# Kernel optimization log

Measured on AMD Instinct MI355X. Metric: run time of the kernel, lower is better.

The kernel has to match this reference:

```python
import jax, jax.numpy as jnp
import numpy as np

NUM_HEADS = 8
MASK_RATE = 0.5


def setup_inputs() -> dict:
    key = jax.random.key(0)
    ks = jax.random.split(key, 6)
    B, N, C = 8, 1024, 256
    TABLE = 10
    att_embedding = jax.random.normal(ks[0], (B, N, C), dtype=jnp.float32)
    relation_position = jax.random.randint(ks[1], (B, N, N), 0, TABLE, dtype=jnp.int32)
    rel_len = jax.random.randint(ks[2], (B,), 0, 20, dtype=jnp.int32)
    W_qkv = jax.random.normal(ks[3], (C, 3 * C), dtype=jnp.float32) * (1.0 / np.sqrt(C))
    W_proj = jax.random.normal(ks[4], (C, C), dtype=jnp.float32) * (1.0 / np.sqrt(C))
    b_proj = jnp.zeros((C,), dtype=jnp.float32)
    bias_table = jax.random.normal(ks[5], (TABLE, NUM_HEADS), dtype=jnp.float32) * 0.02
    return {
        "att_embedding": att_embedding,
        "relation_position": relation_position,
        "rel_len": rel_len,
        "W_qkv": W_qkv,
        "W_proj": W_proj,
        "b_proj": b_proj,
        "bias_table": bias_table,
    }


def reference(att_embedding, relation_position, rel_len, W_qkv, W_proj, b_proj, bias_table):
    B, N, C = att_embedding.shape
    H = NUM_HEADS
    hd = C // H
    scale = hd ** -0.5

    # QKV projection (no bias): [B,N,3C] -> q,k,v each [B,H,N,hd]
    qkv = (att_embedding @ W_qkv).reshape(B, N, 3, H, hd)
    qkv = jnp.transpose(qkv, (2, 0, 3, 1, 4))
    q, k, v = qkv[0], qkv[1], qkv[2]

    # Attention scores [B,H,N,N]
    attn = jnp.einsum("bhnd,bhmd->bhnm", q, k) * scale

    # Relative position bias: gather [B,N,N,H] -> [B,H,N,N]
    pos_bias = jnp.transpose(bias_table[relation_position], (0, 3, 1, 2))

    # Mask bias: table row t gets -100 iff t > mask_len (mask_len+1 .. TABLE-1);
    # identical across heads -> compute as [B,1,N,N] instead of materializing [B,H,N,N].
    mask_len = (rel_len.astype(jnp.float32) * MASK_RATE).astype(jnp.int32)
    mask_bias = jnp.where(relation_position > mask_len[:, None, None], -100.0, 0.0)[:, None]

    attn = jax.nn.softmax(attn + pos_bias + mask_bias, axis=-1)

    # Weighted values -> [B,N,C] -> output projection
    x = jnp.einsum("bhnm,bhmd->bnhd", attn, v).reshape(B, N, C)
    x = x @ W_proj + b_proj
    return x
```

## Files before the change

kernel.cpp:

```cpp
#include <hip/hip_runtime.h>
#include <hip/hip_bf16.h>

typedef __bf16 bf16;
typedef __bf16 bf16x2 __attribute__((ext_vector_type(2)));
typedef __bf16 bf16x8 __attribute__((ext_vector_type(8)));
typedef float f32x4 __attribute__((ext_vector_type(4)));
typedef int i32x4 __attribute__((ext_vector_type(4)));

#define B_ 8
#define N_ 1024
#define C_ 256
#define H_ 8
#define C3_ 768
#define SCALE 0.17677669529663689f
#define FMAX 16.0f


__global__ __launch_bounds__(256) void prep(
    const float* __restrict__ Wqkv, const float* __restrict__ Wproj,
    bf16* __restrict__ Wq_tiled, bf16* __restrict__ Wp_tiled)
{
  int o = blockIdx.x * 256 + threadIdx.x;
  if (blockIdx.x < 768) {
    int k = o / C3_, n = o % C3_;
    float v = Wqkv[o];
    int kt = k >> 5, kk = k & 31, nt = n >> 6, nr = n & 63;
    Wq_tiled[kt * 24576 + nt * 2048 + nr * 32 + kk] = (bf16)v;
  } else {
    int p = o - 768 * 256;
    int k = p >> 8, n = p & 255;
    float v = Wproj[p];
    Wp_tiled[(k >> 5) * 8192 + n * 32 + (k & 31)] = (bf16)v;
  }
}

__global__ __launch_bounds__(256) void gemm_qkv(
    const float* __restrict__ A, const bf16* __restrict__ Wq_tiled,
    bf16* __restrict__ q, bf16* __restrict__ kT, bf16* __restrict__ vT)
{
  __shared__ bf16 As[128][40];
  __shared__ bf16 Bts[128][40];
  __shared__ bf16 Vls[64][136];

  int tid = threadIdx.x;
  int wave = tid >> 6, lane = tid & 63, quad = lane >> 4, l16 = lane & 15;
  int m0 = blockIdx.x * 128, n0 = blockIdx.y * 128;
  int msub = (wave & 1) * 64, nsub = (wave >> 1) * 64;

  f32x4 acc[4][4] = {};

  int arow = tid >> 1, akc = (tid & 1) * 16;
  const float* aptr = A + (long)(m0 + arow) * C_ + akc;
  int bn = tid >> 1, bkc = (tid & 1) * 16;
  const bf16* bptr = Wq_tiled +
      ((long)(blockIdx.y * 2 + (bn >> 6)) * 2048 + (bn & 63) * 32 + bkc);

  float4 a0 = *reinterpret_cast<const float4*>(aptr);
  float4 a1 = *reinterpret_cast<const float4*>(aptr + 4);
  float4 a2 = *reinterpret_cast<const float4*>(aptr + 8);
  float4 a3 = *reinterpret_cast<const float4*>(aptr + 12);
  i32x4 bv0 = *reinterpret_cast<const i32x4*>(bptr);
  i32x4 bv1 = *reinterpret_cast<const i32x4*>(bptr + 8);

  for (int kt = 0; kt < 8; ++kt) {
    __syncthreads();
    {
      bf16 at[16] = {(bf16)a0.x, (bf16)a0.y, (bf16)a0.z, (bf16)a0.w,
                     (bf16)a1.x, (bf16)a1.y, (bf16)a1.z, (bf16)a1.w,
                     (bf16)a2.x, (bf16)a2.y, (bf16)a2.z, (bf16)a2.w,
                     (bf16)a3.x, (bf16)a3.y, (bf16)a3.z, (bf16)a3.w};
      *reinterpret_cast<bf16x8*>(&As[arow][akc]) = *reinterpret_cast<bf16x8*>(at);
      *reinterpret_cast<bf16x8*>(&As[arow][akc + 8]) = *reinterpret_cast<bf16x8*>(at + 8);
      *reinterpret_cast<i32x4*>(&Bts[bn][bkc]) = bv0;
      *reinterpret_cast<i32x4*>(&Bts[bn][bkc + 8]) = bv1;
    }
    __syncthreads();

    if (kt < 7) {
      int kn = (kt + 1) * 32;
      a0 = *reinterpret_cast<const float4*>(aptr + kn);
      a1 = *reinterpret_cast<const float4*>(aptr + kn + 4);
      a2 = *reinterpret_cast<const float4*>(aptr + kn + 8);
      a3 = *reinterpret_cast<const float4*>(aptr + kn + 12);
      bv0 = *reinterpret_cast<const i32x4*>(bptr + (long)(kt + 1) * 24576);
      bv1 = *reinterpret_cast<const i32x4*>(bptr + (long)(kt + 1) * 24576 + 8);
    }

    bf16x8 af[4], bfr[4];
#pragma unroll
    for (int mi = 0; mi < 4; ++mi)
      af[mi] = *reinterpret_cast<const bf16x8*>(&As[msub + mi * 16 + l16][quad * 8]);
#pragma unroll
    for (int ni = 0; ni < 4; ++ni)
      bfr[ni] = *reinterpret_cast<const bf16x8*>(&Bts[nsub + ni * 16 + l16][quad * 8]);
#pragma unroll
    for (int mi = 0; mi < 4; ++mi)
#pragma unroll
      for (int ni = 0; ni < 4; ++ni)
        acc[mi][ni] = __builtin_amdgcn_mfma_f32_16x16x32_bf16(af[mi], bfr[ni], acc[mi][ni], 0, 0, 0);
  }

  if (n0 < 256) {
#pragma unroll
    for (int mi = 0; mi < 4; ++mi)
#pragma unroll
      for (int ni = 0; ni < 4; ++ni)
#pragma unroll
        for (int r = 0; r < 4; ++r) {
          int row = m0 + msub + mi * 16 + quad * 4 + r;
          int col = n0 + nsub + ni * 16 + l16;
          q[(long)row * 256 + col] = (bf16)(acc[mi][ni][r] * SCALE);
        }
  } else if (n0 < 512) {
#pragma unroll
    for (int mi = 0; mi < 4; ++mi)
#pragma unroll
      for (int ni = 0; ni < 4; ++ni)
#pragma unroll
        for (int r = 0; r < 4; ++r) {
          int row = m0 + msub + mi * 16 + quad * 4 + r;
          int c = n0 + nsub + ni * 16 + l16 - 256;
          int b = row >> 10, n = row & 1023;
          int h = c >> 5, d = c & 31;
          kT[(((long)(b * H_ + h)) * N_ + n) * 32 + d] = (bf16)acc[mi][ni][r];
        }
  } else {
    int b = m0 >> 10;
#pragma unroll
    for (int ch = 0; ch < 2; ++ch) {
      __syncthreads();
      if ((nsub >> 6) == ch) {
#pragma unroll
        for (int mi = 0; mi < 4; ++mi)
#pragma unroll
          for (int ni = 0; ni < 4; ++ni)
#pragma unroll
            for (int r = 0; r < 4; ++r) {
              int cc = ni * 16 + l16;
              int nn = msub + mi * 16 + quad * 4 + r;
              int np = (nn & 96) | (2 * (nn & 15)) | ((nn >> 4) & 1);
              Vls[cc][np] = (bf16)acc[mi][ni][r];
            }
      }
      __syncthreads();
      int cc = tid >> 2, nseg = (tid & 3) * 32;
      long base = ((long)(b * C_ + (n0 - 512) + ch * 64 + cc)) * N_ + (m0 & 1023) + nseg;
#pragma unroll
      for (int j = 0; j < 4; ++j)
        *reinterpret_cast<i32x4*>(vT + base + j * 8) =
            *reinterpret_cast<const i32x4*>(&Vls[cc][nseg + j * 8]);
    }
  }
}

__global__ __launch_bounds__(512) void flash_attn(
    const bf16* __restrict__ q, const bf16* __restrict__ kT,
    const bf16* __restrict__ vT, const int* __restrict__ rel,
    const int* __restrict__ rel_len, const float* __restrict__ btab,
    const bf16* __restrict__ Wp_tiled, const float* __restrict__ bias,
    float* __restrict__ out)
{
  __shared__ bf16 Vs[256][40];
  __shared__ unsigned RelsP[4][33];
  __shared__ bf16 Pls[H_][16 * 40];
  __shared__ float btl[H_][16];
  __shared__ bf16 attL[16][264];

  int tid = threadIdx.x;
  int h = tid >> 6, lane = tid & 63, quad = lane >> 4, l16 = lane & 15;
  int b = blockIdx.y, i0 = blockIdx.x * 16;
  long bN = (long)b * N_;

  int mask_len = (int)((float)rel_len[b] * 0.5f);
  if (tid < 80) {
    int t = tid >> 3, hh = tid & 7;
    btl[hh][t] = btab[t * H_ + hh] + (t > mask_len ? -100.f : 0.f) - FMAX;
  }

  bf16x8 qf = *reinterpret_cast<const bf16x8*>(
      q + (bN + i0 + l16) * 256 + h * 32 + quad * 8);

  const bf16* kbase = kT + ((long)(b * H_ + h)) * N_ * 32 + quad * 8;
  int vrow = tid >> 1, voff = (tid & 1) * 16;
  const bf16* vgp = vT + ((long)b * C_ + vrow) * N_ + voff;
  int rg = (tid >> 5) & 3, rcol = tid & 31;
  const int* rgp = rel + (bN + i0 + rg * 4) * N_ + rcol;

  bf16x8 kf0 = *reinterpret_cast<const bf16x8*>(kbase + (long)l16 * 32);
  bf16x8 kf1 = *reinterpret_cast<const bf16x8*>(kbase + (long)(16 + l16) * 32);
  bf16x8 vr0 = *reinterpret_cast<const bf16x8*>(vgp);
  bf16x8 vr1 = *reinterpret_cast<const bf16x8*>(vgp + 8);
  int rr0 = 0, rr1 = 0, rr2 = 0, rr3 = 0;
  if (tid < 128) {
    rr0 = rgp[0]; rr1 = rgp[N_]; rr2 = rgp[2 * N_]; rr3 = rgp[3 * N_];
  }

  f32x4 oacc[2] = {};
  float l_part[4] = {0.f, 0.f, 0.f, 0.f};

  for (int j0 = 0; j0 < N_; j0 += 32) {
    __syncthreads();
    *reinterpret_cast<bf16x8*>(&Vs[vrow][voff]) = vr0;
    *reinterpret_cast<bf16x8*>(&Vs[vrow][voff + 8]) = vr1;
    if (tid < 128)
      RelsP[rg][rcol] = (unsigned)rr0 | ((unsigned)rr1 << 8) |
                        ((unsigned)rr2 << 16) | ((unsigned)rr3 << 24);
    __syncthreads();

    int jn = j0 + 32; jn = (jn < N_) ? jn : 0;
    bf16x8 kn0 = *reinterpret_cast<const bf16x8*>(kbase + (long)(jn + l16) * 32);
    bf16x8 kn1 = *reinterpret_cast<const bf16x8*>(kbase + (long)(jn + 16 + l16) * 32);
    vr0 = *reinterpret_cast<const bf16x8*>(vgp + jn);
    vr1 = *reinterpret_cast<const bf16x8*>(vgp + jn + 8);
    if (tid < 128) {
      rr0 = rgp[jn]; rr1 = rgp[N_ + jn];
      rr2 = rgp[2 * N_ + jn]; rr3 = rgp[3 * N_ + jn];
    }

    f32x4 z = {};
    f32x4 s0 = __builtin_amdgcn_mfma_f32_16x16x32_bf16(qf, kf0, z, 0, 0, 0);
    f32x4 s1 = __builtin_amdgcn_mfma_f32_16x16x32_bf16(qf, kf1, z, 0, 0, 0);
    kf0 = kn0; kf1 = kn1;

    unsigned w0 = RelsP[quad][l16];
    unsigned w1 = RelsP[quad][16 + l16];
#pragma unroll
    for (int r = 0; r < 4; ++r) {
      int il = quad * 4 + r;
      int rv0 = (w0 >> (8 * r)) & 255;
      int rv1 = (w1 >> (8 * r)) & 255;
      float p0 = __expf(s0[r] + btl[h][rv0]);
      float p1 = __expf(s1[r] + btl[h][rv1]);
      l_part[r] += p0 + p1;
      bf16x2 pp = {(bf16)p0, (bf16)p1};
      *reinterpret_cast<bf16x2*>(&Pls[h][il * 40 + l16 * 2]) = pp;
    }
    asm volatile("s_waitcnt lgkmcnt(0)" ::: "memory");
    bf16x8 pf = *reinterpret_cast<const bf16x8*>(&Pls[h][l16 * 40 + quad * 8]);
    bf16x8 vf0 = *reinterpret_cast<const bf16x8*>(&Vs[h * 32 + l16][quad * 8]);
    bf16x8 vf1 = *reinterpret_cast<const bf16x8*>(&Vs[h * 32 + 16 + l16][quad * 8]);
    oacc[0] = __builtin_amdgcn_mfma_f32_16x16x32_bf16(pf, vf0, oacc[0], 0, 0, 0);
    oacc[1] = __builtin_amdgcn_mfma_f32_16x16x32_bf16(pf, vf1, oacc[1], 0, 0, 0);
  }

#pragma unroll
  for (int r = 0; r < 4; ++r) {
    float l = l_part[r];
#pragma unroll
    for (int m = 1; m < 16; m <<= 1) l += __shfl_xor(l, m);
    float inv = 1.f / l;
    attL[quad * 4 + r][h * 32 + l16] = (bf16)(oacc[0][r] * inv);
    attL[quad * 4 + r][h * 32 + 16 + l16] = (bf16)(oacc[1][r] * inv);
  }
  __syncthreads();

  f32x4 pacc[2] = {};
  const bf16* wp = Wp_tiled + ((h * 32 + l16) * 32 + quad * 8);
#pragma unroll
  for (int kt = 0; kt < 8; ++kt) {
    bf16x8 afr = *reinterpret_cast<const bf16x8*>(&attL[l16][kt * 32 + quad * 8]);
    bf16x8 b0 = *reinterpret_cast<const bf16x8*>(wp + kt * 8192);
    bf16x8 b1 = *reinterpret_cast<const bf16x8*>(wp + kt * 8192 + 512);
    pacc[0] = __builtin_amdgcn_mfma_f32_16x16x32_bf16(afr, b0, pacc[0], 0, 0, 0);
    pacc[1] = __builtin_amdgcn_mfma_f32_16x16x32_bf16(afr, b1, pacc[1], 0, 0, 0);
  }
  float bi0 = bias[h * 32 + l16];
  float bi1 = bias[h * 32 + 16 + l16];
#pragma unroll
  for (int r = 0; r < 4; ++r) {
    long rowoff = (bN + i0 + quad * 4 + r) * C_ + h * 32;
    out[rowoff + l16] = pacc[0][r] + bi0;
    out[rowoff + 16 + l16] = pacc[1][r] + bi1;
  }
}

extern "C" void kernel_launch(void* const* d_in, const int* in_sizes, int n_in,
                              void* d_out, int out_size, void* d_ws, size_t ws_size,
                              hipStream_t stream) {
  const float* X     = (const float*)d_in[0];
  const int*   rel   = (const int*)d_in[1];
  const int*   rlen  = (const int*)d_in[2];
  const float* Wqkv  = (const float*)d_in[3];
  const float* Wproj = (const float*)d_in[4];
  const float* bproj = (const float*)d_in[5];
  const float* btab  = (const float*)d_in[6];
  float* out = (float*)d_out;

  char* ws = (char*)d_ws;
  bf16* Wq_tiled = (bf16*)ws;
  bf16* Wp_tiled = (bf16*)(ws + 393216);
  bf16* q  = (bf16*)(ws + 524288);
  bf16* kT = (bf16*)(ws + 524288 + 4194304);
  bf16* vT = (bf16*)(ws + 524288 + 2 * 4194304);

  prep<<<dim3(1024), 256, 0, stream>>>(Wqkv, Wproj, Wq_tiled, Wp_tiled);
  gemm_qkv<<<dim3(8192 / 128, C3_ / 128), 256, 0, stream>>>(X, Wq_tiled, q, kT, vT);
  flash_attn<<<dim3(N_ / 16, B_), 512, 0, stream>>>(
      q, kT, vT, rel, rlen, btab, Wp_tiled, bproj, out);
}
```

Before: 142.6 us.

## Split attention key range across two wave groups per block and merge partials

Doubles the flash_attn block to 1024 threads. Each group of eight waves covers one half of the key sequence, using its own V and relation tiles in shared memory, and the partial outputs and row sums are combined through shared memory before normalization. The output projection is then spread across all 16 waves, each handling 16 columns. The goal is shorter per-block serial loop latency and more waves in flight, at the cost of extra shared memory, a reduction step and more barriers.

```diff
diff --git a/kernel.cpp b/kernel.cpp
--- a/kernel.cpp
+++ b/kernel.cpp
@@ -153,23 +153,26 @@
   }
 }
 
-__global__ __launch_bounds__(512) void flash_attn(
+__global__ __launch_bounds__(1024) void flash_attn(
     const bf16* __restrict__ q, const bf16* __restrict__ kT,
     const bf16* __restrict__ vT, const int* __restrict__ rel,
     const int* __restrict__ rel_len, const float* __restrict__ btab,
     const bf16* __restrict__ Wp_tiled, const float* __restrict__ bias,
     float* __restrict__ out)
 {
-  __shared__ bf16 Vs[256][40];
-  __shared__ unsigned RelsP[4][33];
-  __shared__ bf16 Pls[H_][16 * 40];
+  __shared__ bf16 Vs[2][256][40];
+  __shared__ unsigned RelsP[2][4][33];
+  __shared__ bf16 Pls[16][16 * 40];
   __shared__ float btl[H_][16];
   __shared__ bf16 attL[16][264];
 
   int tid = threadIdx.x;
-  int h = tid >> 6, lane = tid & 63, quad = lane >> 4, l16 = lane & 15;
+  int w = tid >> 6, h = w & 7, jh = w >> 3;
+  int lane = tid & 63, quad = lane >> 4, l16 = lane & 15;
   int b = blockIdx.y, i0 = blockIdx.x * 16;
   long bN = (long)b * N_;
+  int jbase = jh * 512;
+  int ht = tid & 511;
 
   int mask_len = (int)((float)rel_len[b] * 0.5f);
   if (tid < 80) {
@@ -181,40 +184,40 @@
       q + (bN + i0 + l16) * 256 + h * 32 + quad * 8);
 
   const bf16* kbase = kT + ((long)(b * H_ + h)) * N_ * 32 + quad * 8;
-  int vrow = tid >> 1, voff = (tid & 1) * 16;
-  const bf16* vgp = vT + ((long)b * C_ + vrow) * N_ + voff;
-  int rg = (tid >> 5) & 3, rcol = tid & 31;
-  const int* rgp = rel + (bN + i0 + rg * 4) * N_ + rcol;
-
-  bf16x8 kf0 = *reinterpret_cast<const bf16x8*>(kbase + (long)l16 * 32);
-  bf16x8 kf1 = *reinterpret_cast<const bf16x8*>(kbase + (long)(16 + l16) * 32);
+  int vrow = ht >> 1, voff = (ht & 1) * 16;
+  const bf16* vgp = vT + ((long)b * C_ + vrow) * N_ + voff + jbase;
+  int rg = (ht >> 5) & 3, rcol = ht & 31;
+  const int* rgp = rel + (bN + i0 + rg * 4) * N_ + rcol + jbase;
+
+  bf16x8 kf0 = *reinterpret_cast<const bf16x8*>(kbase + (long)(jbase + l16) * 32);
+  bf16x8 kf1 = *reinterpret_cast<const bf16x8*>(kbase + (long)(jbase + 16 + l16) * 32);
   bf16x8 vr0 = *reinterpret_cast<const bf16x8*>(vgp);
   bf16x8 vr1 = *reinterpret_cast<const bf16x8*>(vgp + 8);
   int rr0 = 0, rr1 = 0, rr2 = 0, rr3 = 0;
-  if (tid < 128) {
+  if (ht < 128) {
     rr0 = rgp[0]; rr1 = rgp[N_]; rr2 = rgp[2 * N_]; rr3 = rgp[3 * N_];
   }
 
   f32x4 oacc[2] = {};
   float l_part[4] = {0.f, 0.f, 0.f, 0.f};
 
-  for (int j0 = 0; j0 < N_; j0 += 32) {
+  for (int jt = 0; jt < 16; ++jt) {
     __syncthreads();
-    *reinterpret_cast<bf16x8*>(&Vs[vrow][voff]) = vr0;
-    *reinterpret_cast<bf16x8*>(&Vs[vrow][voff + 8]) = vr1;
-    if (tid < 128)
-      RelsP[rg][rcol] = (unsigned)rr0 | ((unsigned)rr1 << 8) |
-                        ((unsigned)rr2 << 16) | ((unsigned)rr3 << 24);
+    *reinterpret_cast<bf16x8*>(&Vs[jh][vrow][voff]) = vr0;
+    *reinterpret_cast<bf16x8*>(&Vs[jh][vrow][voff + 8]) = vr1;
+    if (ht < 128)
+      RelsP[jh][rg][rcol] = (unsigned)rr0 | ((unsigned)rr1 << 8) |
+                            ((unsigned)rr2 << 16) | ((unsigned)rr3 << 24);
     __syncthreads();
 
-    int jn = j0 + 32; jn = (jn < N_) ? jn : 0;
-    bf16x8 kn0 = *reinterpret_cast<const bf16x8*>(kbase + (long)(jn + l16) * 32);
-    bf16x8 kn1 = *reinterpret_cast<const bf16x8*>(kbase + (long)(jn + 16 + l16) * 32);
-    vr0 = *reinterpret_cast<const bf16x8*>(vgp + jn);
-    vr1 = *reinterpret_cast<const bf16x8*>(vgp + jn + 8);
-    if (tid < 128) {
-      rr0 = rgp[jn]; rr1 = rgp[N_ + jn];
-      rr2 = rgp[2 * N_ + jn]; rr3 = rgp[3 * N_ + jn];
+    int jo = (jt < 15) ? (jt + 1) * 32 : 0;
+    bf16x8 kn0 = *reinterpret_cast<const bf16x8*>(kbase + (long)(jbase + jo + l16) * 32);
+    bf16x8 kn1 = *reinterpret_cast<const bf16x8*>(kbase + (long)(jbase + jo + 16 + l16) * 32);
+    vr0 = *reinterpret_cast<const bf16x8*>(vgp + jo);
+    vr1 = *reinterpret_cast<const bf16x8*>(vgp + jo + 8);
+    if (ht < 128) {
+      rr0 = rgp[jo]; rr1 = rgp[N_ + jo];
+      rr2 = rgp[2 * N_ + jo]; rr3 = rgp[3 * N_ + jo];
     }
 
     f32x4 z = {};
@@ -222,8 +225,8 @@
     f32x4 s1 = __builtin_amdgcn_mfma_f32_16x16x32_bf16(qf, kf1, z, 0, 0, 0);
     kf0 = kn0; kf1 = kn1;
 
-    unsigned w0 = RelsP[quad][l16];
-    unsigned w1 = RelsP[quad][16 + l16];
+    unsigned w0 = RelsP[jh][quad][l16];
+    unsigned w1 = RelsP[jh][quad][16 + l16];
 #pragma unroll
     for (int r = 0; r < 4; ++r) {
       int il = quad * 4 + r;
@@ -233,44 +236,61 @@
       float p1 = __expf(s1[r] + btl[h][rv1]);
       l_part[r] += p0 + p1;
       bf16x2 pp = {(bf16)p0, (bf16)p1};
-      *reinterpret_cast<bf16x2*>(&Pls[h][il * 40 + l16 * 2]) = pp;
+      *reinterpret_cast<bf16x2*>(&Pls[w][il * 40 + l16 * 2]) = pp;
     }
     asm volatile("s_waitcnt lgkmcnt(0)" ::: "memory");
-    bf16x8 pf = *reinterpret_cast<const bf16x8*>(&Pls[h][l16 * 40 + quad * 8]);
-    bf16x8 vf0 = *reinterpret_cast<const bf16x8*>(&Vs[h * 32 + l16][quad * 8]);
-    bf16x8 vf1 = *reinterpret_cast<const bf16x8*>(&Vs[h * 32 + 16 + l16][quad * 8]);
+    bf16x8 pf = *reinterpret_cast<const bf16x8*>(&Pls[w][l16 * 40 + quad * 8]);
+    bf16x8 vf0 = *reinterpret_cast<const bf16x8*>(&Vs[jh][h * 32 + l16][quad * 8]);
+    bf16x8 vf1 = *reinterpret_cast<const bf16x8*>(&Vs[jh][h * 32 + 16 + l16][quad * 8]);
     oacc[0] = __builtin_amdgcn_mfma_f32_16x16x32_bf16(pf, vf0, oacc[0], 0, 0, 0);
     oacc[1] = __builtin_amdgcn_mfma_f32_16x16x32_bf16(pf, vf1, oacc[1], 0, 0, 0);
   }
 
-#pragma unroll
-  for (int r = 0; r < 4; ++r) {
-    float l = l_part[r];
-#pragma unroll
-    for (int m = 1; m < 16; m <<= 1) l += __shfl_xor(l, m);
-    float inv = 1.f / l;
-    attL[quad * 4 + r][h * 32 + l16] = (bf16)(oacc[0][r] * inv);
-    attL[quad * 4 + r][h * 32 + 16 + l16] = (bf16)(oacc[1][r] * inv);
-  }
   __syncthreads();
-
-  f32x4 pacc[2] = {};
-  const bf16* wp = Wp_tiled + ((h * 32 + l16) * 32 + quad * 8);
+  float* scr = reinterpret_cast<float*>(&Vs[0][0][0]);
+  if (jh == 1) {
+    int base = (h * 64 + lane) * 12;
+#pragma unroll
+    for (int r = 0; r < 4; ++r) {
+      scr[base + r] = oacc[0][r];
+      scr[base + 4 + r] = oacc[1][r];
+      scr[base + 8 + r] = l_part[r];
+    }
+  }
+  __syncthreads();
+  if (jh == 0) {
+    int base = (h * 64 + lane) * 12;
+#pragma unroll
+    for (int r = 0; r < 4; ++r) {
+      oacc[0][r] += scr[base + r];
+      oacc[1][r] += scr[base + 4 + r];
+      l_part[r] += scr[base + 8 + r];
+    }
+#pragma unroll
+    for (int r = 0; r < 4; ++r) {
+      float l = l_part[r];
+#pragma unroll
+      for (int m = 1; m < 16; m <<= 1) l += __shfl_xor(l, m);
+      float inv = 1.f / l;
+      attL[quad * 4 + r][h * 32 + l16] = (bf16)(oacc[0][r] * inv);
+      attL[quad * 4 + r][h * 32 + 16 + l16] = (bf16)(oacc[1][r] * inv);
+    }
+  }
+  __syncthreads();
+
+  f32x4 pacc = {};
+  const bf16* wp = Wp_tiled + ((w * 16 + l16) * 32 + quad * 8);
 #pragma unroll
   for (int kt = 0; kt < 8; ++kt) {
     bf16x8 afr = *reinterpret_cast<const bf16x8*>(&attL[l16][kt * 32 + quad * 8]);
-    bf16x8 b0 = *reinterpret_cast<const bf16x8*>(wp + kt * 8192);
-    bf16x8 b1 = *reinterpret_cast<const bf16x8*>(wp + kt * 8192 + 512);
-    pacc[0] = __builtin_amdgcn_mfma_f32_16x16x32_bf16(afr, b0, pacc[0], 0, 0, 0);
-    pacc[1] = __builtin_amdgcn_mfma_f32_16x16x32_bf16(afr, b1, pacc[1], 0, 0, 0);
-  }
-  float bi0 = bias[h * 32 + l16];
-  float bi1 = bias[h * 32 + 16 + l16];
+    bf16x8 bfr = *reinterpret_cast<const bf16x8*>(wp + kt * 8192);
+    pacc = __builtin_amdgcn_mfma_f32_16x16x32_bf16(afr, bfr, pacc, 0, 0, 0);
+  }
+  float bi = bias[w * 16 + l16];
 #pragma unroll
   for (int r = 0; r < 4; ++r) {
-    long rowoff = (bN + i0 + quad * 4 + r) * C_ + h * 32;
-    out[rowoff + l16] = pacc[0][r] + bi0;
-    out[rowoff + 16 + l16] = pacc[1][r] + bi1;
+    long rowoff = (bN + i0 + quad * 4 + r) * C_ + w * 16;
+    out[rowoff + l16] = pacc[r] + bi;
   }
 }
 
@@ -295,6 +315,6 @@
 
   prep<<<dim3(1024), 256, 0, stream>>>(Wqkv, Wproj, Wq_tiled, Wp_tiled);
   gemm_qkv<<<dim3(8192 / 128, C3_ / 128), 256, 0, stream>>>(X, Wq_tiled, q, kT, vT);
-  flash_attn<<<dim3(N_ / 16, B_), 512, 0, stream>>>(
+  flash_attn<<<dim3(N_ / 16, B_), 1024, 0, stream>>>(
       q, kT, vT, rel, rlen, btab, Wp_tiled, bproj, out);
 }
```

New measurement: 155.1 us. 8.8% more time.
